# Kernel tuning notes

Hardware: AMD Instinct MI355X
Metric: run time of the kernel (lower is better)

Reference implementation:

```python
import jax, jax.numpy as jnp
import numpy as np


def setup_inputs() -> dict:
    key = jax.random.key(0)
    k1, k2 = jax.random.split(key)
    N, C, D, Hg, Wg = 2, 12, 8, 16, 16
    H, W = 1024, 1024
    grid = jax.random.normal(k1, (N, C, D, Hg, Wg), dtype=jnp.float32)
    guidemap = jax.random.uniform(k2, (N, 1, H, W), dtype=jnp.float32)
    return {"grid": grid, "guidemap": guidemap}


def reference(grid, guidemap):
    # Bilateral grid slicing: 3D trilinear grid_sample, padding='border', align_corners=True.
    # grid: [N, C, D, Hg, Wg]; guidemap: [N, 1, H, W] -> out: [N, C, H, W]
    N, C, D, Hg, Wg = grid.shape
    _, _, H, W = guidemap.shape

    # Normalized sample coords in [-1, 1] (meshgrid over output pixels).
    yn = jnp.linspace(-1.0, 1.0, H)                      # [H]
    xn = jnp.linspace(-1.0, 1.0, W)                      # [W]
    zn = guidemap[:, 0] * 2.0 - 1.0                      # [N, H, W]

    # Unnormalize (align_corners=True) and clamp to border.
    iy = jnp.clip((yn + 1.0) * 0.5 * (Hg - 1), 0.0, Hg - 1.0)  # [H]
    ix = jnp.clip((xn + 1.0) * 0.5 * (Wg - 1), 0.0, Wg - 1.0)  # [W]
    iz = jnp.clip((zn + 1.0) * 0.5 * (D - 1), 0.0, D - 1.0)    # [N, H, W]

    iy0 = jnp.floor(iy).astype(jnp.int32)
    ix0 = jnp.floor(ix).astype(jnp.int32)
    iy1 = jnp.minimum(iy0 + 1, Hg - 1)
    ix1 = jnp.minimum(ix0 + 1, Wg - 1)
    wy = (iy - iy0)[:, None]                              # [H, 1]
    wx = (ix - ix0)[None, :]                              # [1, W]

    Y0, Y1 = iy0[:, None], iy1[:, None]                   # [H, 1]
    X0, X1 = ix0[None, :], ix1[None, :]                   # [1, W]

    iz0 = jnp.floor(iz).astype(jnp.int32)                 # [N, H, W]
    iz1 = jnp.minimum(iz0 + 1, D - 1)
    wz = iz - iz0                                         # [N, H, W]

    def sample_one(g, z0, z1, wzn):
        # g: [C, D, Hg, Wg]; z0, z1, wzn: [H, W]
        def gat(zz, yy, xx):
            return g[:, zz, yy, xx]                       # [C, H, W]
        # interpolate along z first, then x, then y
        c00 = gat(z0, Y0, X0) * (1.0 - wzn) + gat(z1, Y0, X0) * wzn
        c01 = gat(z0, Y0, X1) * (1.0 - wzn) + gat(z1, Y0, X1) * wzn
        c10 = gat(z0, Y1, X0) * (1.0 - wzn) + gat(z1, Y1, X0) * wzn
        c11 = gat(z0, Y1, X1) * (1.0 - wzn) + gat(z1, Y1, X1) * wzn
        c0 = c00 * (1.0 - wx) + c01 * wx
        c1 = c10 * (1.0 - wx) + c11 * wx
        return c0 * (1.0 - wy) + c1 * wy                  # [C, H, W]

    coeff = jax.vmap(sample_one)(grid, iz0, iz1, wz)      # [N, C, H, W]
    return coeff
```

## Files before the change

### kernel.cpp

```cpp
#include <hip/hip_runtime.h>

#define H 1024
#define W 1024
#define NC 12
#define ND 8
#define HG 16
#define WG 16
#define ROWS 2
#define PX 2
#define HALFW 512
#define XPITCH 100

__global__ __launch_bounds__(256, 6) void slice_kernel(
    const float* __restrict__ grid,
    const float* __restrict__ guide,
    float* __restrict__ out)
{
    const int xh  = blockIdx.x & 1;
    const int yp  = blockIdx.x >> 1;
    const int n   = blockIdx.y;
    const int y0  = yp * ROWS;
    const int tid = threadIdx.x;
    const int xb  = xh * HALFW + tid * PX;

    const float* gd = guide + ((size_t)n * H + y0) * W;
    float2 g2[ROWS];
    g2[0] = *(const float2*)&gd[xb];
    g2[1] = *(const float2*)&gd[W + xb];

    __shared__ __align__(16) float sg[ROWS][WG * XPITCH];
    const float* gbase = grid + (size_t)n * NC * ND * HG * WG;

    #pragma unroll
    for (int r = 0; r < ROWS; ++r) {
        const int y = y0 + r;
        float yn = -1.0f + (float)y * (2.0f / (float)(H - 1));
        float iy = (yn + 1.0f) * 0.5f * (float)(HG - 1);
        iy = fminf(fmaxf(iy, 0.0f), (float)(HG - 1));
        int   iy0 = (int)floorf(iy);
        int   iy1 = min(iy0 + 1, HG - 1);
        float wy  = iy - (float)iy0;

        #pragma unroll
        for (int k = 0; k < (WG * ND * NC) / 256; ++k) {
            int i  = tid + k * 256;
            int x  = i & (WG - 1);
            int zc = i >> 4;
            int z  = zc & (ND - 1);
            int c  = zc >> 3;
            const float* gp = gbase + ((c * ND + z) * HG) * WG + x;
            float r0 = gp[iy0 * WG];
            float r1 = gp[iy1 * WG];
            sg[r][x * XPITCH + z * NC + c] = r0 + (r1 - r0) * wy;
        }
    }

    int   B0[PX], B1[PX];
    float wxv[PX];
    #pragma unroll
    for (int p = 0; p < PX; ++p) {
        const int x = xb + p;
        float xn = -1.0f + (float)x * (2.0f / (float)(W - 1));
        float ix = (xn + 1.0f) * 0.5f * (float)(WG - 1);
        ix = fminf(fmaxf(ix, 0.0f), (float)(WG - 1));
        int   ix0 = (int)floorf(ix);
        int   ix1 = min(ix0 + 1, WG - 1);
        wxv[p] = ix - (float)ix0;
        B0[p]  = ix0 * XPITCH;
        B1[p]  = ix1 * XPITCH;
    }

    __syncthreads();

    float* ob = out + (size_t)n * NC * H * W + (size_t)y0 * W + xb;

    #pragma unroll
    for (int r = 0; r < ROWS; ++r) {
        const float gz[PX] = { g2[r].x, g2[r].y };

        int   A00[PX], A01[PX], A10[PX], A11[PX];
        float w00[PX], w01[PX], w10[PX], w11[PX];
        #pragma unroll
        for (int p = 0; p < PX; ++p) {
            float zn = gz[p] * 2.0f - 1.0f;
            float iz = (zn + 1.0f) * 0.5f * (float)(ND - 1);
            iz = fminf(fmaxf(iz, 0.0f), (float)(ND - 1));
            int   iz0 = (int)floorf(iz);
            int   iz1 = min(iz0 + 1, ND - 1);
            float wz  = iz - (float)iz0;

            const int Z0 = iz0 * NC;
            const int Z1 = iz1 * NC;
            A00[p] = B0[p] + Z0;  A01[p] = B0[p] + Z1;
            A10[p] = B1[p] + Z0;  A11[p] = B1[p] + Z1;

            const float wx = wxv[p];
            const float ux = 1.0f - wx;
            const float uz = 1.0f - wz;
            w00[p] = ux * uz;  w01[p] = ux * wz;
            w10[p] = wx * uz;  w11[p] = wx * wz;
        }

        #pragma unroll
        for (int cc = 0; cc < NC; cc += 4) {
            float4 q[PX];
            #pragma unroll
            for (int p = 0; p < PX; ++p) {
                const float4 a0 = *(const float4*)&sg[r][A00[p] + cc];
                const float4 a1 = *(const float4*)&sg[r][A01[p] + cc];
                const float4 b0 = *(const float4*)&sg[r][A10[p] + cc];
                const float4 b1 = *(const float4*)&sg[r][A11[p] + cc];
                const float k00 = w00[p], k01 = w01[p], k10 = w10[p], k11 = w11[p];
                q[p].x = a0.x * k00 + a1.x * k01 + b0.x * k10 + b1.x * k11;
                q[p].y = a0.y * k00 + a1.y * k01 + b0.y * k10 + b1.y * k11;
                q[p].z = a0.z * k00 + a1.z * k01 + b0.z * k10 + b1.z * k11;
                q[p].w = a0.w * k00 + a1.w * k01 + b0.w * k10 + b1.w * k11;
            }
            {
                float2 v;
                v = make_float2(q[0].x, q[1].x);
                *(float2*)&ob[(size_t)(cc + 0) * H * W + (size_t)r * W] = v;
                v = make_float2(q[0].y, q[1].y);
                *(float2*)&ob[(size_t)(cc + 1) * H * W + (size_t)r * W] = v;
                v = make_float2(q[0].z, q[1].z);
                *(float2*)&ob[(size_t)(cc + 2) * H * W + (size_t)r * W] = v;
                v = make_float2(q[0].w, q[1].w);
                *(float2*)&ob[(size_t)(cc + 3) * H * W + (size_t)r * W] = v;
            }
        }
    }
}

extern "C" void kernel_launch(void* const* d_in, const int* in_sizes, int n_in,
                              void* d_out, int out_size, void* d_ws, size_t ws_size,
                              hipStream_t stream) {
    const float* grid  = (const float*)d_in[0];
    const float* guide = (const float*)d_in[1];
    float* out = (float*)d_out;

    dim3 grd((W / HALFW) * (H / ROWS), 2);
    dim3 blk(256);
    slice_kernel<<<grd, blk, 0, stream>>>(grid, guide, out);
}
```

Measured before the change: 119.6 us.

## Give each wavefront its own slab, drop block sync, use 16B nontemporal stores

Each wavefront now builds its own y-interpolated grid slab in shared memory for one half-row and then consumes it, so the block-wide __syncthreads is removed. Each thread processes 4 pixels and writes 16-byte nontemporal stores instead of 8-byte stores, and the coordinate arithmetic is simplified to single scale factors. The cost is duplicated slab construction: each wavefront loads and interpolates the full slab for its half-row, and the larger shared-memory and register footprint lowers the occupancy hint from 6 to 4. The code also relies on intra-wavefront ordering between the shared-memory writes and reads, since no barrier remains.

```diff
diff --git a/kernel.cpp b/kernel.cpp
--- a/kernel.cpp
+++ b/kernel.cpp
@@ -6,95 +6,85 @@
 #define ND 8
 #define HG 16
 #define WG 16
-#define ROWS 2
-#define PX 2
-#define HALFW 512
-#define XPITCH 100
+#define CELL (ND * NC)
+#define SLAB (WG * CELL)
+#define HWSZ (H * W)
 
-__global__ __launch_bounds__(256, 6) void slice_kernel(
+typedef float f32x4 __attribute__((ext_vector_type(4)));
+
+__global__ __launch_bounds__(256, 4) void slice_kernel(
     const float* __restrict__ grid,
     const float* __restrict__ guide,
     float* __restrict__ out)
 {
-    const int xh  = blockIdx.x & 1;
-    const int yp  = blockIdx.x >> 1;
+    const int tid = threadIdx.x;
+    const int wv  = tid >> 6;
+    const int ln  = tid & 63;
     const int n   = blockIdx.y;
-    const int y0  = yp * ROWS;
-    const int tid = threadIdx.x;
-    const int xb  = xh * HALFW + tid * PX;
+    const int y   = blockIdx.x * 2 + (wv >> 1);
+    const int xw  = (wv & 1) * 512;
 
-    const float* gd = guide + ((size_t)n * H + y0) * W;
-    float2 g2[ROWS];
-    g2[0] = *(const float2*)&gd[xb];
-    g2[1] = *(const float2*)&gd[W + xb];
+    __shared__ __align__(16) float sg[4][SLAB];
+    float* S = sg[wv];
 
-    __shared__ __align__(16) float sg[ROWS][WG * XPITCH];
-    const float* gbase = grid + (size_t)n * NC * ND * HG * WG;
+    const float* gd = guide + ((size_t)n * H + y) * W + xw;
+    const float4 ga = *(const float4*)&gd[ln * 4];
+    const float4 gb = *(const float4*)&gd[256 + ln * 4];
 
+    float iy = fminf((float)y * (15.0f / 1023.0f), 15.0f);
+    const int   iy0 = (int)iy;
+    const int   iy1 = min(iy0 + 1, HG - 1);
+    const float wy  = iy - (float)iy0;
+
+    const float* gslab = grid + (size_t)n * (NC * ND * HG * WG);
+    const int lx = ln >> 4;
+    const int lm = ln & 15;
     #pragma unroll
-    for (int r = 0; r < ROWS; ++r) {
-        const int y = y0 + r;
-        float yn = -1.0f + (float)y * (2.0f / (float)(H - 1));
-        float iy = (yn + 1.0f) * 0.5f * (float)(HG - 1);
-        iy = fminf(fmaxf(iy, 0.0f), (float)(HG - 1));
-        int   iy0 = (int)floorf(iy);
-        int   iy1 = min(iy0 + 1, HG - 1);
-        float wy  = iy - (float)iy0;
-
+    for (int K = 0; K < 6; ++K) {
+        const int m = lm + (K << 4);
+        const int z = (m * 171) >> 11;
+        const int c = m - z * 12;
+        const float* gp = gslab + (size_t)((c * ND + z) * HG) * WG;
+        const float* g0 = gp + iy0 * WG;
+        const float* g1 = gp + iy1 * WG;
         #pragma unroll
-        for (int k = 0; k < (WG * ND * NC) / 256; ++k) {
-            int i  = tid + k * 256;
-            int x  = i & (WG - 1);
-            int zc = i >> 4;
-            int z  = zc & (ND - 1);
-            int c  = zc >> 3;
-            const float* gp = gbase + ((c * ND + z) * HG) * WG + x;
-            float r0 = gp[iy0 * WG];
-            float r1 = gp[iy1 * WG];
-            sg[r][x * XPITCH + z * NC + c] = r0 + (r1 - r0) * wy;
+        for (int j = 0; j < 4; ++j) {
+            const int k = (K << 2) + j;
+            const int x = ((k << 2) + lx) & 15;
+            const float r0 = g0[x];
+            const float r1 = g1[x];
+            S[x * CELL + m] = r0 + (r1 - r0) * wy;
         }
     }
 
-    int   B0[PX], B1[PX];
-    float wxv[PX];
-    #pragma unroll
-    for (int p = 0; p < PX; ++p) {
-        const int x = xb + p;
-        float xn = -1.0f + (float)x * (2.0f / (float)(W - 1));
-        float ix = (xn + 1.0f) * 0.5f * (float)(WG - 1);
-        ix = fminf(fmaxf(ix, 0.0f), (float)(WG - 1));
-        int   ix0 = (int)floorf(ix);
-        int   ix1 = min(ix0 + 1, WG - 1);
-        wxv[p] = ix - (float)ix0;
-        B0[p]  = ix0 * XPITCH;
-        B1[p]  = ix1 * XPITCH;
-    }
-
-    __syncthreads();
-
-    float* ob = out + (size_t)n * NC * H * W + (size_t)y0 * W + xb;
+    float* obase = out + ((size_t)n * NC * H + y) * W;
 
     #pragma unroll
-    for (int r = 0; r < ROWS; ++r) {
-        const float gz[PX] = { g2[r].x, g2[r].y };
+    for (int ch = 0; ch < 2; ++ch) {
+        const float4 g  = ch ? gb : ga;
+        const int    xb = xw + ch * 256 + (ln << 2);
+        const float gz4[4] = { g.x, g.y, g.z, g.w };
 
-        int   A00[PX], A01[PX], A10[PX], A11[PX];
-        float w00[PX], w01[PX], w10[PX], w11[PX];
+        int   A00[4], A01[4], A10[4], A11[4];
+        float w00[4], w01[4], w10[4], w11[4];
         #pragma unroll
-        for (int p = 0; p < PX; ++p) {
-            float zn = gz[p] * 2.0f - 1.0f;
-            float iz = (zn + 1.0f) * 0.5f * (float)(ND - 1);
-            iz = fminf(fmaxf(iz, 0.0f), (float)(ND - 1));
-            int   iz0 = (int)floorf(iz);
-            int   iz1 = min(iz0 + 1, ND - 1);
-            float wz  = iz - (float)iz0;
+        for (int p = 0; p < 4; ++p) {
+            const int x = xb + p;
+            float ix = fminf((float)x * (15.0f / 1023.0f), 15.0f);
+            const int   ix0 = (int)ix;
+            const int   ix1 = min(ix0 + 1, WG - 1);
+            const float wx  = ix - (float)ix0;
 
-            const int Z0 = iz0 * NC;
-            const int Z1 = iz1 * NC;
-            A00[p] = B0[p] + Z0;  A01[p] = B0[p] + Z1;
-            A10[p] = B1[p] + Z0;  A11[p] = B1[p] + Z1;
+            float iz = fminf(fmaxf(gz4[p] * 7.0f, 0.0f), 7.0f);
+            const int   iz0 = (int)iz;
+            const int   iz1 = min(iz0 + 1, ND - 1);
+            const float wz  = iz - (float)iz0;
 
-            const float wx = wxv[p];
+            A00[p] = ix0 * CELL + iz0 * NC;
+            A01[p] = ix0 * CELL + iz1 * NC;
+            A10[p] = ix1 * CELL + iz0 * NC;
+            A11[p] = ix1 * CELL + iz1 * NC;
+
             const float ux = 1.0f - wx;
             const float uz = 1.0f - wz;
             w00[p] = ux * uz;  w01[p] = ux * wz;
@@ -103,30 +93,28 @@
 
         #pragma unroll
         for (int cc = 0; cc < NC; cc += 4) {
-            float4 q[PX];
+            float4 q[4];
             #pragma unroll
-            for (int p = 0; p < PX; ++p) {
-                const float4 a0 = *(const float4*)&sg[r][A00[p] + cc];
-                const float4 a1 = *(const float4*)&sg[r][A01[p] + cc];
-                const float4 b0 = *(const float4*)&sg[r][A10[p] + cc];
-                const float4 b1 = *(const float4*)&sg[r][A11[p] + cc];
+            for (int p = 0; p < 4; ++p) {
+                const float4 a0 = *(const float4*)&S[A00[p] + cc];
+                const float4 a1 = *(const float4*)&S[A01[p] + cc];
+                const float4 b0 = *(const float4*)&S[A10[p] + cc];
+                const float4 b1 = *(const float4*)&S[A11[p] + cc];
                 const float k00 = w00[p], k01 = w01[p], k10 = w10[p], k11 = w11[p];
                 q[p].x = a0.x * k00 + a1.x * k01 + b0.x * k10 + b1.x * k11;
                 q[p].y = a0.y * k00 + a1.y * k01 + b0.y * k10 + b1.y * k11;
                 q[p].z = a0.z * k00 + a1.z * k01 + b0.z * k10 + b1.z * k11;
                 q[p].w = a0.w * k00 + a1.w * k01 + b0.w * k10 + b1.w * k11;
             }
-            {
-                float2 v;
-                v = make_float2(q[0].x, q[1].x);
-                *(float2*)&ob[(size_t)(cc + 0) * H * W + (size_t)r * W] = v;
-                v = make_float2(q[0].y, q[1].y);
-                *(float2*)&ob[(size_t)(cc + 1) * H * W + (size_t)r * W] = v;
-                v = make_float2(q[0].z, q[1].z);
-                *(float2*)&ob[(size_t)(cc + 2) * H * W + (size_t)r * W] = v;
-                v = make_float2(q[0].w, q[1].w);
-                *(float2*)&ob[(size_t)(cc + 3) * H * W + (size_t)r * W] = v;
-            }
+            f32x4 v;
+            v = (f32x4){ q[0].x, q[1].x, q[2].x, q[3].x };
+            __builtin_nontemporal_store(v, (f32x4*)&obase[(size_t)(cc + 0) * HWSZ + xb]);
+            v = (f32x4){ q[0].y, q[1].y, q[2].y, q[3].y };
+            __builtin_nontemporal_store(v, (f32x4*)&obase[(size_t)(cc + 1) * HWSZ + xb]);
+            v = (f32x4){ q[0].z, q[1].z, q[2].z, q[3].z };
+            __builtin_nontemporal_store(v, (f32x4*)&obase[(size_t)(cc + 2) * HWSZ + xb]);
+            v = (f32x4){ q[0].w, q[1].w, q[2].w, q[3].w };
+            __builtin_nontemporal_store(v, (f32x4*)&obase[(size_t)(cc + 3) * HWSZ + xb]);
         }
     }
 }
@@ -138,7 +126,7 @@
     const float* guide = (const float*)d_in[1];
     float* out = (float*)d_out;
 
-    dim3 grd((W / HALFW) * (H / ROWS), 2);
+    dim3 grd(H / 2, 2);
     dim3 blk(256);
     slice_kernel<<<grd, blk, 0, stream>>>(grid, guide, out);
 }
```

Result: slower. 141.4 us (+18.2%).
